# Kernel optimization log

Measured on AMD Instinct MI355X. Metric: run time of the kernel, lower is better.

The kernel has to match this reference:

```python
import jax, jax.numpy as jnp
import numpy as np

IN = 128; HID = 128; OUT = 128; HEADS = 3; T1 = 0.2; T2 = 0.2
B = 512; L = 32; V = 100000; NMETA = 5


def _corr_full(s, t):
    # s, t: (B, L, E, N). Full cross-correlation along last axis.
    # Matches F.conv1d(hs, ht, groups=BLE, padding=N-1): out[k] = sum_m s[k+m-(N-1)] * t[m]
    N = s.shape[-1]
    sp = jnp.pad(s, ((0, 0), (0, 0), (0, 0), (N - 1, N - 1)))
    out = jnp.stack([(sp[..., k:k + N] * t).sum(-1) for k in range(2 * N - 1)], axis=-1)
    return jnp.swapaxes(out, -1, -2)  # (B, L, 2N-1, E)


def _node_att(h, Wt, Ws, Wc):
    # h: (B, L, P, E); Wt/Ws/Wc: (HEADS, E, HID)
    Bh, Lh, P, E = h.shape
    H = h.reshape(Bh * Lh, P, E)
    hi = jnp.einsum('ne,heo->hno', H[:, 0], Wt)                 # target-node projection
    logits = jnp.einsum('npe,heo,hno->hnp', H, Ws, hi) / T1     # (heads, BL, P)
    alpha = jax.nn.softmax(logits, axis=-1)                     # softmax over path positions
    Z = jnp.einsum('hnp,npe,heo->no', alpha, H, Wc) / HEADS     # mean over heads
    return Z.reshape(Bh, Lh, -1)


def _forward(emb_user, emb_item, emb_attr1, emb_attr2, emb_attr3, Wt, Ws, Wc,
             pw1, pb1, pw2, fw1, fb1, fw2, fb2,
             UI, IU, UIUI, IUIU, UIAI1, IAIU1, UIAI2, IAIU2, UIAI3, IAIU3):
    src = emb_user[UI[:, 0, 0]]
    tgt = emb_item[IU[:, 0, 0]]
    ui = jnp.stack([emb_user[UI[..., 0]], emb_item[UI[..., 1]]], axis=3)
    iu = jnp.stack([emb_item[IU[..., 0]], emb_user[IU[..., 1]]], axis=3)

    def p4(tabs, idx):
        return jnp.stack([tabs[k][idx[..., k]] for k in range(4)], axis=3)

    uiui = p4([emb_user, emb_item, emb_user, emb_item], UIUI)
    iuiu = p4([emb_item, emb_user, emb_item, emb_user], IUIU)
    uiai1 = p4([emb_user, emb_item, emb_attr1, emb_item], UIAI1)
    iaiu1 = p4([emb_item, emb_attr1, emb_item, emb_user], IAIU1)
    uiai2 = p4([emb_user, emb_item, emb_attr2, emb_item], UIAI2)
    iaiu2 = p4([emb_item, emb_attr2, emb_item, emb_user], IAIU2)
    uiai3 = p4([emb_user, emb_item, emb_attr3, emb_item], UIAI3)
    iaiu3 = p4([emb_item, emb_attr3, emb_item, emb_user], IAIU3)

    user_feats = [ui, uiui, uiai1, uiai2, uiai3]
    item_feats = [iu, iuiu, iaiu1, iaiu2, iaiu3]
    Hs = [_node_att(_corr_full(uf, itf), Wt[m], Ws[m], Wc[m])
          for m, (uf, itf) in enumerate(zip(user_feats, item_feats))]
    Z = jnp.stack(Hs, 1)                        # (B, 5, L, HID)
    z = Z.reshape(Z.shape[0], -1, HID)          # (B, 5L, HID)
    w = jnp.tanh(z @ pw1 + pb1) @ pw2 / T2      # (B, 5L, 1)
    beta = jax.nn.softmax(w, axis=1)
    path_out = (beta * z).sum(1)                # (B, HID)
    x = jnp.concatenate([src, tgt, path_out], axis=1)
    x = jax.nn.relu(x @ fw1 + fb1)              # dropout in eval mode -> identity
    return jax.nn.sigmoid(x @ fw2 + fb2)        # (B, 1)


def setup_inputs() -> dict:
    key = jax.random.key(0)
    ks = jax.random.split(key, 24)

    def idx(k, n):
        return jax.random.randint(k, (B, L, n), 0, V, dtype=jnp.int32)

    d = {
        'UI': idx(ks[0], 2), 'IU': idx(ks[1], 2),
        'UIUI': idx(ks[2], 4), 'IUIU': idx(ks[3], 4),
        'UIAI1': idx(ks[4], 4), 'IAIU1': idx(ks[5], 4),
        'UIAI2': idx(ks[6], 4), 'IAIU2': idx(ks[7], 4),
        'UIAI3': idx(ks[8], 4), 'IAIU3': idx(ks[9], 4),
    }

    def emb(k):
        t = jax.random.normal(k, (V + 1, IN), jnp.float32) * 0.05
        return t.at[0].set(0.0)  # padding_idx=0

    d['emb_user'] = emb(ks[10]); d['emb_item'] = emb(ks[11])
    d['emb_attr1'] = emb(ks[12]); d['emb_attr2'] = emb(ks[13]); d['emb_attr3'] = emb(ks[14])
    s = (2.0 / (IN + HID)) ** 0.5  # xavier scale
    d['Wt'] = jax.random.normal(ks[15], (NMETA, HEADS, IN, HID), jnp.float32) * s
    d['Ws'] = jax.random.normal(ks[16], (NMETA, HEADS, IN, HID), jnp.float32) * s
    d['Wc'] = jax.random.normal(ks[17], (NMETA, HEADS, IN, HID), jnp.float32) * s
    d['pw1'] = jax.random.normal(ks[18], (HID, HID), jnp.float32) * s
    d['pb1'] = jnp.zeros((HID,), jnp.float32)
    d['pw2'] = jax.random.normal(ks[19], (HID, 1), jnp.float32) * s
    d['fw1'] = jax.random.normal(ks[20], (3 * HID, OUT), jnp.float32) * 0.02
    d['fb1'] = jnp.zeros((OUT,), jnp.float32)
    d['fw2'] = jax.random.normal(ks[21], (OUT, 1), jnp.float32) * 0.02
    d['fb2'] = jnp.zeros((1,), jnp.float32)
    return d


def reference(UI, IU, UIUI, IUIU, UIAI1, IAIU1, UIAI2, IAIU2, UIAI3, IAIU3,
              emb_user, emb_item, emb_attr1, emb_attr2, emb_attr3,
              Wt, Ws, Wc, pw1, pb1, pw2, fw1, fb1, fw2, fb2):
    return _forward(emb_user, emb_item, emb_attr1, emb_attr2, emb_attr3, Wt, Ws, Wc,
                    pw1, pb1, pw2, fw1, fb1, fw2, fb2,
                    UI, IU, UIUI, IUIU, UIAI1, IAIU1, UIAI2, IAIU2, UIAI3, IAIU3)
```

## Files before the change

### kernel.cpp

```cpp
#include <hip/hip_runtime.h>
#include <hip/hip_bf16.h>
#include <cstdint>
#include <cstddef>


typedef __hip_bfloat16 bf16;
typedef __attribute__((ext_vector_type(8))) short  bfrag;
typedef __attribute__((ext_vector_type(4))) float  ffrag;

#define NNODES 16384

__device__ __forceinline__ float bflo(uint32_t u) { return __uint_as_float(u << 16); }
__device__ __forceinline__ float bfhi(uint32_t u) { return __uint_as_float(u & 0xffff0000u); }
__device__ __forceinline__ float bfs(short s) {
  return __uint_as_float(((uint32_t)(unsigned short)s) << 16);
}
__device__ __forceinline__ uint16_t f2bfu(float x) {
  bf16 h = __float2bfloat16(x);
  return *(uint16_t*)&h;
}
__device__ __forceinline__ uint32_t pk2(float lo, float hi) {
  return (uint32_t)f2bfu(lo) | ((uint32_t)f2bfu(hi) << 16);
}

__global__ __launch_bounds__(256) void prep_all(
    const float* __restrict__ Ws, const float* __restrict__ Wt,
    const float* __restrict__ Wc, const float* __restrict__ pw1,
    bf16* __restrict__ BmT, bf16* __restrict__ WcT, bf16* __restrict__ pw1T)
{
  int bid = blockIdx.x;
  int tid = threadIdx.x;
  if (bid < 240) {
    int mh = bid >> 4;
    int g  = bid & 15;
    int m = mh / 3, h = mh % 3;
    const float* ws = Ws + (size_t)mh * 16384;
    const float* wt = Wt + (size_t)mh * 16384;
    int e = tid & 127, half = tid >> 7;
    __shared__ float wtl[2][128];
    for (int ep0 = g * 8; ep0 < g * 8 + 8; ep0 += 2) {
      int ep = ep0 + half;
      wtl[half][e] = wt[ep * 128 + e];
      __syncthreads();
      float acc = 0.f;
      #pragma unroll 4
      for (int o = 0; o < 128; ++o) acc += ws[e * 128 + o] * wtl[half][o];
      BmT[((size_t)(m * 384 + h * 128 + e)) * 128 + ep] = __float2bfloat16(acc);
      __syncthreads();
    }
  } else if (bid < 1200) {
    int idx = (bid - 240) * 256 + tid;
    int he = idx % 384, mo = idx / 384;
    int m = mo >> 7, o = mo & 127;
    WcT[idx] = __float2bfloat16(Wc[((size_t)m * 384 + he) * 128 + o]);
  } else {
    int idx = (bid - 1200) * 256 + tid;
    int o = idx >> 7, k = idx & 127;
    pw1T[idx] = __float2bfloat16(pw1[(size_t)k * 128 + o]);
  }
}

template <int P>
__device__ __forceinline__ void metapath_body(
    char* smem,
    const float* __restrict__ Tu0, const float* __restrict__ Tu1,
    const float* __restrict__ Tu2, const float* __restrict__ Tu3,
    const float* __restrict__ Tt0, const float* __restrict__ Tt1,
    const float* __restrict__ Tt2, const float* __restrict__ Tt3,
    const int* __restrict__ idxU, const int* __restrict__ idxT,
    const bf16* __restrict__ BmT,
    const bf16* __restrict__ WcT,
    bf16* __restrict__ Zall, int m, int tile)
{
  constexpr int PP = 2 * P - 1;
  constexpr int NS = PP * 136;
  bf16* Hs = (bf16*)smem;
  bf16* Ss = Hs + 16 * NS;
  bf16* Al = Ss + 16 * 392;

  int tid = threadIdx.x;
  int lane = tid & 63, wid = tid >> 6;
  int l15 = lane & 15, l4 = lane >> 4;
  int n0 = tile * 16;

  {
    const float* TU[4] = {Tu0, Tu1, Tu2, Tu3};
    const float* TT[4] = {Tt0, Tt1, Tt2, Tt3};
    int e = tid & 127;
    float su[4][P], st[4][P];
    #pragma unroll
    for (int g = 0; g < 4; ++g) {
      int n = n0 + g * 4 + (tid >> 7);
      #pragma unroll
      for (int p = 0; p < P; ++p) {
        su[g][p] = TU[p][(size_t)idxU[n * P + p] * 128 + e];
        st[g][p] = TT[p][(size_t)idxT[n * P + p] * 128 + e];
      }
    }
    #pragma unroll
    for (int g = 0; g < 4; ++g) {
      int ln = g * 4 + (tid >> 7);
      bf16* Hn = &Hs[ln * NS + e];
      #pragma unroll
      for (int k = 0; k < PP; ++k) {
        float acc = 0.f;
        #pragma unroll
        for (int i = 0; i < P; ++i) {
          int j = k + i - (P - 1);
          if (j >= 0 && j < P) acc += su[g][j] * st[g][i];
        }
        Hn[k * 136] = __float2bfloat16(acc);
      }
    }
  }
  __syncthreads();

  {
    bfrag a[4];
    #pragma unroll
    for (int kk = 0; kk < 4; ++kk)
      a[kk] = *(const bfrag*)&Hs[l15 * NS + kk * 32 + 8 * l4];
    #pragma unroll
    for (int f = 0; f < 3; ++f) {
      int col = wid * 48 + f * 16 + l15;
      ffrag acc = {0.f, 0.f, 0.f, 0.f};
      #pragma unroll
      for (int kk = 0; kk < 4; ++kk) {
        bfrag b = *(const bfrag*)&BmT[(size_t)col * 128 + kk * 32 + 8 * l4];
        acc = __builtin_amdgcn_mfma_f32_16x16x32_bf16(a[kk], b, acc, 0, 0, 0);
      }
      #pragma unroll
      for (int r = 0; r < 4; ++r) {
        int node = 4 * l4 + r;
        Ss[node * 392 + col] = __float2bfloat16(acc[r]);
      }
    }
  }
  __syncthreads();

  {
    int nd0 = wid * 2, nd1 = nd0 + 1;
    bool hi = (l15 >= 8);
    int nodeA = hi ? nd1 : nd0;
    int r15 = hi ? (l15 - 8) : l15;
    int ah = (r15 < 3) ? r15 : 2;
    int bp = (r15 < PP) ? r15 : (PP - 1);
    ffrag lacc = {0.f, 0.f, 0.f, 0.f};
    #pragma unroll
    for (int kk = 0; kk < 4; ++kk) {
      bfrag av = *(const bfrag*)&Ss[nodeA * 392 + ah * 128 + kk * 32 + 8 * l4];
      bfrag bv = *(const bfrag*)&Hs[nodeA * NS + bp * 136 + kk * 32 + 8 * l4];
      lacc = __builtin_amdgcn_mfma_f32_16x16x32_bf16(av, bv, lacc, 0, 0, 0);
    }
    bool val = ((l4 == 0) && !hi && (l15 < PP)) ||
               ((l4 == 2) &&  hi && (r15 < PP));
    float lg0 = val ? lacc[0] * 5.0f : -1e30f;
    float lg1 = val ? lacc[1] * 5.0f : -1e30f;
    float lg2 = val ? lacc[2] * 5.0f : -1e30f;
    float m0 = lg0, m1 = lg1, m2 = lg2;
    #pragma unroll
    for (int d = 1; d < 8; d <<= 1) {
      m0 = fmaxf(m0, __shfl_xor(m0, d));
      m1 = fmaxf(m1, __shfl_xor(m1, d));
      m2 = fmaxf(m2, __shfl_xor(m2, d));
    }
    float e0 = val ? __expf(lg0 - m0) : 0.f;
    float e1 = val ? __expf(lg1 - m1) : 0.f;
    float e2 = val ? __expf(lg2 - m2) : 0.f;
    float s0 = e0, s1 = e1, s2 = e2;
    #pragma unroll
    for (int d = 1; d < 8; d <<= 1) {
      s0 += __shfl_xor(s0, d);
      s1 += __shfl_xor(s1, d);
      s2 += __shfl_xor(s2, d);
    }
    if (val) {
      bf16* Aln = Al + nodeA * 24;
      Aln[r15]      = __float2bfloat16(e0 / s0);
      Aln[8 + r15]  = __float2bfloat16(e1 / s1);
      Aln[16 + r15] = __float2bfloat16(e2 / s2);
    }

    int node = tid >> 5, q = tid & 31;
    bfrag al0 = *(const bfrag*)&Al[node * 24];
    bfrag al1 = *(const bfrag*)&Al[node * 24 + 8];
    bfrag al2 = *(const bfrag*)&Al[node * 24 + 16];
    #pragma unroll
    for (int j = 0; j < 2; ++j) {
      int e2i = 4 * q + 2 * j;
      float a00 = 0.f, a01 = 0.f, a10 = 0.f, a11 = 0.f, a20 = 0.f, a21 = 0.f;
      #pragma unroll
      for (int pp = 0; pp < PP; ++pp) {
        uint32_t hv = *(const uint32_t*)&Hs[node * NS + pp * 136 + e2i];
        float lo = bflo(hv), hh = bfhi(hv);
        float f0 = bfs(al0[pp]);
        float f1 = bfs(al1[pp]);
        float f2 = bfs(al2[pp]);
        a00 += f0 * lo; a01 += f0 * hh;
        a10 += f1 * lo; a11 += f1 * hh;
        a20 += f2 * lo; a21 += f2 * hh;
      }
      *(uint32_t*)&Ss[node * 392 +       e2i] = pk2(a00, a01);
      *(uint32_t*)&Ss[node * 392 + 128 + e2i] = pk2(a10, a11);
      *(uint32_t*)&Ss[node * 392 + 256 + e2i] = pk2(a20, a21);
    }
  }
  __syncthreads();

  {
    bfrag a[12];
    #pragma unroll
    for (int kk = 0; kk < 12; ++kk)
      a[kk] = *(const bfrag*)&Ss[l15 * 392 + kk * 32 + 8 * l4];
    int col = wid * 16 + l15;
    ffrag acc = {0.f, 0.f, 0.f, 0.f};
    #pragma unroll
    for (int kk = 0; kk < 12; ++kk) {
      bfrag b = *(const bfrag*)&WcT[(size_t)col * 384 + kk * 32 + 8 * l4];
      acc = __builtin_amdgcn_mfma_f32_16x16x32_bf16(a[kk], b, acc, 0, 0, 0);
    }
    #pragma unroll
    for (int r = 0; r < 4; ++r) {
      int gn = n0 + 4 * l4 + r;
      int crow = (((gn >> 5) * 5 + m) << 5) + (gn & 31);
      Zall[(size_t)crow * 128 + col] = __float2bfloat16(acc[r] * (1.0f / 3.0f));
    }
  }
}

__global__ __launch_bounds__(512) void fused_all(
    const float* __restrict__ emb_user, const float* __restrict__ emb_item,
    const float* __restrict__ emb_a1, const float* __restrict__ emb_a2,
    const float* __restrict__ emb_a3,
    const int* __restrict__ UI,    const int* __restrict__ IU,
    const int* __restrict__ UIUI,  const int* __restrict__ IUIU,
    const int* __restrict__ UIAI1, const int* __restrict__ IAIU1,
    const int* __restrict__ UIAI2, const int* __restrict__ IAIU2,
    const int* __restrict__ UIAI3, const int* __restrict__ IAIU3,
    const bf16* __restrict__ BmT, const bf16* __restrict__ WcT,
    bf16* __restrict__ Zall)
{
  extern __shared__ char smem[];
  int bid = blockIdx.x;
  int m = bid >> 10, tile = bid & 1023;
  if (m == 0) {
    metapath_body<2>(smem, emb_user, emb_item, nullptr, nullptr,
                     emb_item, emb_user, nullptr, nullptr,
                     UI, IU, BmT, WcT, Zall, 0, tile);
  } else {
    const float* u2 = (m == 1) ? emb_user : (m == 2) ? emb_a1
                    : (m == 3) ? emb_a2 : emb_a3;
    const int* iu_ = (m == 1) ? UIUI : (m == 2) ? UIAI1
                   : (m == 3) ? UIAI2 : UIAI3;
    const int* it_ = (m == 1) ? IUIU : (m == 2) ? IAIU1
                   : (m == 3) ? IAIU2 : IAIU3;
    metapath_body<4>(smem, emb_user, emb_item, u2, emb_item,
                     emb_item, u2, emb_item, emb_user,
                     iu_, it_,
                     BmT + (size_t)m * 49152, WcT + (size_t)m * 49152,
                     Zall, m, tile);
  }
}

__global__ __launch_bounds__(512) void fused_tail(
    const bf16* __restrict__ Zall,
    const bf16* __restrict__ pw1T,
    const float* __restrict__ pb1, const float* __restrict__ pw2,
    const int* __restrict__ UI, const int* __restrict__ IU,
    const float* __restrict__ emb_user, const float* __restrict__ emb_item,
    const float* __restrict__ fw1, const float* __restrict__ fb1,
    const float* __restrict__ fw2, const float* __restrict__ fb2,
    float* __restrict__ out)
{
  __shared__ bf16 Zs[160 * 136];
  __shared__ float wrow[160];
  __shared__ float ph[4][128];
  __shared__ float xs[384];
  __shared__ float sred[16];
  __shared__ float yred[2];

  int b = blockIdx.x, tid = threadIdx.x;
  int lane = tid & 63, wid = tid >> 6;
  int l15 = lane & 15, l4 = lane >> 4;

  {
    const float4* src = (const float4*)(Zall + (size_t)b * 160 * 128);
    float4 v[5];
    #pragma unroll
    for (int i = 0; i < 5; ++i) v[i] = src[i * 512 + tid];
    #pragma unroll
    for (int i = 0; i < 5; ++i) {
      int idx = i * 512 + tid;
      int row = idx >> 4, c8 = idx & 15;
      *(float4*)&Zs[row * 136 + c8 * 8] = v[i];
    }
  }
  __syncthreads();

  for (int rf = wid; rf < 10; rf += 8) {
    bfrag a[4];
    #pragma unroll
    for (int kk = 0; kk < 4; ++kk)
      a[kk] = *(const bfrag*)&Zs[(rf * 16 + l15) * 136 + kk * 32 + 8 * l4];
    float part[4] = {0.f, 0.f, 0.f, 0.f};
    #pragma unroll
    for (int f = 0; f < 8; ++f) {
      int col = f * 16 + l15;
      ffrag acc = {0.f, 0.f, 0.f, 0.f};
      #pragma unroll
      for (int kk = 0; kk < 4; ++kk) {
        bfrag bv = *(const bfrag*)&pw1T[(size_t)col * 128 + kk * 32 + 8 * l4];
        acc = __builtin_amdgcn_mfma_f32_16x16x32_bf16(a[kk], bv, acc, 0, 0, 0);
      }
      float bias = pb1[col], w2 = pw2[col];
      #pragma unroll
      for (int r = 0; r < 4; ++r) part[r] += tanhf(acc[r] + bias) * w2;
    }
    #pragma unroll
    for (int d = 1; d < 16; d <<= 1) {
      #pragma unroll
      for (int r = 0; r < 4; ++r) part[r] += __shfl_xor(part[r], d);
    }
    if (l15 == 0) {
      #pragma unroll
      for (int r = 0; r < 4; ++r)
        wrow[rf * 16 + 4 * l4 + r] = part[r] * 5.0f;
    }
  }
  __syncthreads();

  {
    float v = (tid < 160) ? wrow[tid] : -1e30f;
    #pragma unroll
    for (int off = 32; off; off >>= 1) v = fmaxf(v, __shfl_xor(v, off));
    if (lane == 0) sred[wid] = v;
    __syncthreads();
    if (tid < 64) {
      float mval = (lane < 8) ? sred[lane] : -1e30f;
      #pragma unroll
      for (int off = 4; off; off >>= 1) mval = fmaxf(mval, __shfl_xor(mval, off));
      if (lane == 0) sred[8] = mval;
    }
    __syncthreads();
    float mx = sred[8];
    float ev = (tid < 160) ? __expf(wrow[tid] - mx) : 0.f;
    float s = ev;
    #pragma unroll
    for (int off = 32; off; off >>= 1) s += __shfl_xor(s, off);
    if (lane == 0) sred[wid] = s;
    __syncthreads();
    if (tid < 64) {
      float sval = (lane < 8) ? sred[lane] : 0.f;
      #pragma unroll
      for (int off = 4; off; off >>= 1) sval += __shfl_xor(sval, off);
      if (lane == 0) sred[9] = sval;
    }
    __syncthreads();
    if (tid < 160) wrow[tid] = ev / sred[9];
  }
  __syncthreads();

  {
    int e = tid & 127, q = tid >> 7;
    float acc = 0.f;
    #pragma unroll 4
    for (int j = q * 40; j < q * 40 + 40; ++j)
      acc += wrow[j] * __bfloat162float(Zs[j * 136 + e]);
    ph[q][e] = acc;
  }
  __syncthreads();

  {
    int su = UI[b * 64];
    int ti = IU[b * 64];
    if (tid < 128) {
      xs[256 + tid] = ph[0][tid] + ph[1][tid] + ph[2][tid] + ph[3][tid];
    } else if (tid < 256) {
      xs[tid - 128] = emb_user[(size_t)su * 128 + (tid - 128)];
    } else if (tid < 384) {
      xs[tid - 128] = emb_item[(size_t)ti * 128 + (tid - 256)];
    }
  }
  __syncthreads();

  {
    int o = tid & 127, q = tid >> 7;
    float acc = 0.f;
    #pragma unroll 4
    for (int i = q * 96; i < q * 96 + 96; ++i)
      acc += xs[i] * fw1[(size_t)i * 128 + o];
    __syncthreads();
    ph[q][o] = acc;
  }
  __syncthreads();
  if (tid < 128) {
    float y = fmaxf(ph[0][tid] + ph[1][tid] + ph[2][tid] + ph[3][tid] + fb1[tid],
                    0.0f) * fw2[tid];
    #pragma unroll
    for (int off = 32; off; off >>= 1) y += __shfl_down(y, off);
    if ((tid & 63) == 0) yred[tid >> 6] = y;
  }
  __syncthreads();
  if (tid == 0) {
    float s = yred[0] + yred[1] + fb2[0];
    out[b] = 1.0f / (1.0f + expf(-s));
  }
}

extern "C" void kernel_launch(void* const* d_in, const int* in_sizes, int n_in,
                              void* d_out, int out_size, void* d_ws, size_t ws_size,
                              hipStream_t stream)
{
  const int* UI    = (const int*)d_in[0];
  const int* IU    = (const int*)d_in[1];
  const int* UIUI  = (const int*)d_in[2];
  const int* IUIU  = (const int*)d_in[3];
  const int* UIAI1 = (const int*)d_in[4];
  const int* IAIU1 = (const int*)d_in[5];
  const int* UIAI2 = (const int*)d_in[6];
  const int* IAIU2 = (const int*)d_in[7];
  const int* UIAI3 = (const int*)d_in[8];
  const int* IAIU3 = (const int*)d_in[9];
  const float* emb_user = (const float*)d_in[10];
  const float* emb_item = (const float*)d_in[11];
  const float* emb_a1   = (const float*)d_in[12];
  const float* emb_a2   = (const float*)d_in[13];
  const float* emb_a3   = (const float*)d_in[14];
  const float* Wt  = (const float*)d_in[15];
  const float* Ws  = (const float*)d_in[16];
  const float* Wc  = (const float*)d_in[17];
  const float* pw1 = (const float*)d_in[18];
  const float* pb1 = (const float*)d_in[19];
  const float* pw2 = (const float*)d_in[20];
  const float* fw1 = (const float*)d_in[21];
  const float* fb1 = (const float*)d_in[22];
  const float* fw2 = (const float*)d_in[23];
  const float* fb2 = (const float*)d_in[24];
  float* out = (float*)d_out;

  char* wsb = (char*)d_ws;
  bf16*  BmT  = (bf16*)wsb;
  bf16*  WcT  = (bf16*)(wsb + 491520);
  bf16*  pw1T = (bf16*)(wsb + 983040);
  bf16*  Zall = (bf16*)(wsb + 1015808);

  prep_all<<<1264, 256, 0, stream>>>(Ws, Wt, Wc, pw1, BmT, WcT, pw1T);

  fused_all<<<5120, 512, 43776, stream>>>(
      emb_user, emb_item, emb_a1, emb_a2, emb_a3,
      UI, IU, UIUI, IUIU, UIAI1, IAIU1, UIAI2, IAIU2, UIAI3, IAIU3,
      BmT, WcT, Zall);

  fused_tail<<<512, 512, 0, stream>>>(Zall, pw1T, pb1, pw2,
                                      UI, IU, emb_user, emb_item,
                                      fw1, fb1, fw2, fb2, out);
}
```

Baseline: 201.8 us.

## Gather bf16 copies of user/item tables and fuse semantic scoring into main kernel

Adds a pre-pass kernel that converts the user and item embedding tables to bf16 on every call. The main metapath kernel then gathers half-width rows for those tables, while the attribute tables stay fp32. The main kernel also computes the per-row semantic-attention score (pw1 projection, tanh, pw2 dot) right after producing each Z tile, writing it to a buffer, so the tail kernel no longer runs that MFMA pass. The trade-off is a full streaming read and write of two large tables every call, plus extra rounding of the embeddings before the correlation.

```diff
diff --git a/kernel.cpp b/kernel.cpp
--- a/kernel.cpp
+++ b/kernel.cpp
@@ -8,12 +8,10 @@
 typedef __attribute__((ext_vector_type(8))) short  bfrag;
 typedef __attribute__((ext_vector_type(4))) float  ffrag;
 
-#define NNODES 16384
-
 __device__ __forceinline__ float bflo(uint32_t u) { return __uint_as_float(u << 16); }
 __device__ __forceinline__ float bfhi(uint32_t u) { return __uint_as_float(u & 0xffff0000u); }
-__device__ __forceinline__ float bfs(short s) {
-  return __uint_as_float(((uint32_t)(unsigned short)s) << 16);
+__device__ __forceinline__ float bfs(unsigned short s) {
+  return __uint_as_float(((uint32_t)s) << 16);
 }
 __device__ __forceinline__ uint16_t f2bfu(float x) {
   bf16 h = __float2bfloat16(x);
@@ -21,6 +19,22 @@
 }
 __device__ __forceinline__ uint32_t pk2(float lo, float hi) {
   return (uint32_t)f2bfu(lo) | ((uint32_t)f2bfu(hi) << 16);
+}
+
+__global__ __launch_bounds__(256) void conv_emb(
+    const float* __restrict__ a, const float* __restrict__ b,
+    ushort* __restrict__ da, ushort* __restrict__ db, int n4)
+{
+  int stride = gridDim.x * 256;
+  for (int i = blockIdx.x * 256 + threadIdx.x; i < 2 * n4; i += stride) {
+    const float4* s; ushort* d; int j;
+    if (i < n4) { s = (const float4*)a; d = da; j = i; }
+    else        { s = (const float4*)b; d = db; j = i - n4; }
+    float4 v = s[j];
+    ushort4 o;
+    o.x = f2bfu(v.x); o.y = f2bfu(v.y); o.z = f2bfu(v.z); o.w = f2bfu(v.w);
+    ((ushort4*)d)[j] = o;
+  }
 }
 
 __global__ __launch_bounds__(256) void prep_all(
@@ -60,23 +74,24 @@
   }
 }
 
-template <int P>
+template <int P, int UM, int TM>
 __device__ __forceinline__ void metapath_body(
     char* smem,
-    const float* __restrict__ Tu0, const float* __restrict__ Tu1,
-    const float* __restrict__ Tu2, const float* __restrict__ Tu3,
-    const float* __restrict__ Tt0, const float* __restrict__ Tt1,
-    const float* __restrict__ Tt2, const float* __restrict__ Tt3,
+    const void* Tu0, const void* Tu1, const void* Tu2, const void* Tu3,
+    const void* Tt0, const void* Tt1, const void* Tt2, const void* Tt3,
     const int* __restrict__ idxU, const int* __restrict__ idxT,
     const bf16* __restrict__ BmT,
     const bf16* __restrict__ WcT,
-    bf16* __restrict__ Zall, int m, int tile)
+    const bf16* __restrict__ pw1T,
+    const float* __restrict__ pb1, const float* __restrict__ pw2,
+    bf16* __restrict__ Zall, float* __restrict__ wbuf, int m, int tile)
 {
   constexpr int PP = 2 * P - 1;
   constexpr int NS = PP * 136;
   bf16* Hs = (bf16*)smem;
   bf16* Ss = Hs + 16 * NS;
   bf16* Al = Ss + 16 * 392;
+  float* wred = (float*)(Al + 16 * 24);
 
   int tid = threadIdx.x;
   int lane = tid & 63, wid = tid >> 6;
@@ -84,8 +99,8 @@
   int n0 = tile * 16;
 
   {
-    const float* TU[4] = {Tu0, Tu1, Tu2, Tu3};
-    const float* TT[4] = {Tt0, Tt1, Tt2, Tt3};
+    const void* TU[4] = {Tu0, Tu1, Tu2, Tu3};
+    const void* TT[4] = {Tt0, Tt1, Tt2, Tt3};
     int e = tid & 127;
     float su[4][P], st[4][P];
     #pragma unroll
@@ -93,8 +108,12 @@
       int n = n0 + g * 4 + (tid >> 7);
       #pragma unroll
       for (int p = 0; p < P; ++p) {
-        su[g][p] = TU[p][(size_t)idxU[n * P + p] * 128 + e];
-        st[g][p] = TT[p][(size_t)idxT[n * P + p] * 128 + e];
+        size_t ou = (size_t)idxU[n * P + p] * 128 + e;
+        size_t ot = (size_t)idxT[n * P + p] * 128 + e;
+        su[g][p] = ((UM >> p) & 1) ? ((const float*)TU[p])[ou]
+                                   : bfs(((const ushort*)TU[p])[ou]);
+        st[g][p] = ((TM >> p) & 1) ? ((const float*)TT[p])[ot]
+                                   : bfs(((const ushort*)TT[p])[ot]);
       }
     }
     #pragma unroll
@@ -193,9 +212,9 @@
       for (int pp = 0; pp < PP; ++pp) {
         uint32_t hv = *(const uint32_t*)&Hs[node * NS + pp * 136 + e2i];
         float lo = bflo(hv), hh = bfhi(hv);
-        float f0 = bfs(al0[pp]);
-        float f1 = bfs(al1[pp]);
-        float f2 = bfs(al2[pp]);
+        float f0 = bfs((unsigned short)al0[pp]);
+        float f1 = bfs((unsigned short)al1[pp]);
+        float f2 = bfs((unsigned short)al2[pp]);
         a00 += f0 * lo; a01 += f0 * hh;
         a10 += f1 * lo; a11 += f1 * hh;
         a20 += f2 * lo; a21 += f2 * hh;
@@ -207,6 +226,7 @@
   }
   __syncthreads();
 
+  bf16* Zs = Hs;
   {
     bfrag a[12];
     #pragma unroll
@@ -221,15 +241,55 @@
     }
     #pragma unroll
     for (int r = 0; r < 4; ++r) {
-      int gn = n0 + 4 * l4 + r;
+      int node = 4 * l4 + r;
+      int gn = n0 + node;
       int crow = (((gn >> 5) * 5 + m) << 5) + (gn & 31);
-      Zall[(size_t)crow * 128 + col] = __float2bfloat16(acc[r] * (1.0f / 3.0f));
-    }
+      bf16 zb = __float2bfloat16(acc[r] * (1.0f / 3.0f));
+      Zall[(size_t)crow * 128 + col] = zb;
+      Zs[node * 136 + col] = zb;
+    }
+  }
+  __syncthreads();
+
+  {
+    bfrag a5[4];
+    #pragma unroll
+    for (int kk = 0; kk < 4; ++kk)
+      a5[kk] = *(const bfrag*)&Zs[l15 * 136 + kk * 32 + 8 * l4];
+    int col = wid * 16 + l15;
+    ffrag acc5 = {0.f, 0.f, 0.f, 0.f};
+    #pragma unroll
+    for (int kk = 0; kk < 4; ++kk) {
+      bfrag b = *(const bfrag*)&pw1T[(size_t)col * 128 + kk * 32 + 8 * l4];
+      acc5 = __builtin_amdgcn_mfma_f32_16x16x32_bf16(a5[kk], b, acc5, 0, 0, 0);
+    }
+    float bias = pb1[col], w2 = pw2[col];
+    float part[4];
+    #pragma unroll
+    for (int r = 0; r < 4; ++r) part[r] = tanhf(acc5[r] + bias) * w2;
+    #pragma unroll
+    for (int d = 1; d < 16; d <<= 1) {
+      #pragma unroll
+      for (int r = 0; r < 4; ++r) part[r] += __shfl_xor(part[r], d);
+    }
+    if (l15 == 0) {
+      #pragma unroll
+      for (int r = 0; r < 4; ++r) wred[wid * 16 + 4 * l4 + r] = part[r];
+    }
+  }
+  __syncthreads();
+  if (tid < 16) {
+    float s = 0.f;
+    #pragma unroll
+    for (int w = 0; w < 8; ++w) s += wred[w * 16 + tid];
+    int gn = n0 + tid;
+    int crow = (((gn >> 5) * 5 + m) << 5) + (gn & 31);
+    wbuf[crow] = s * 5.0f;
   }
 }
 
 __global__ __launch_bounds__(512) void fused_all(
-    const float* __restrict__ emb_user, const float* __restrict__ emb_item,
+    const ushort* __restrict__ EU, const ushort* __restrict__ EI,
     const float* __restrict__ emb_a1, const float* __restrict__ emb_a2,
     const float* __restrict__ emb_a3,
     const int* __restrict__ UI,    const int* __restrict__ IU,
@@ -238,34 +298,39 @@
     const int* __restrict__ UIAI2, const int* __restrict__ IAIU2,
     const int* __restrict__ UIAI3, const int* __restrict__ IAIU3,
     const bf16* __restrict__ BmT, const bf16* __restrict__ WcT,
-    bf16* __restrict__ Zall)
+    const bf16* __restrict__ pw1T,
+    const float* __restrict__ pb1, const float* __restrict__ pw2,
+    bf16* __restrict__ Zall, float* __restrict__ wbuf)
 {
   extern __shared__ char smem[];
   int bid = blockIdx.x;
   int m = bid >> 10, tile = bid & 1023;
   if (m == 0) {
-    metapath_body<2>(smem, emb_user, emb_item, nullptr, nullptr,
-                     emb_item, emb_user, nullptr, nullptr,
-                     UI, IU, BmT, WcT, Zall, 0, tile);
+    metapath_body<2, 0, 0>(smem, EU, EI, nullptr, nullptr,
+                           EI, EU, nullptr, nullptr,
+                           UI, IU, BmT, WcT, pw1T, pb1, pw2,
+                           Zall, wbuf, 0, tile);
+  } else if (m == 1) {
+    metapath_body<4, 0, 0>(smem, EU, EI, EU, EI,
+                           EI, EU, EI, EU,
+                           UIUI, IUIU,
+                           BmT + (size_t)1 * 49152, WcT + (size_t)1 * 49152,
+                           pw1T, pb1, pw2, Zall, wbuf, 1, tile);
   } else {
-    const float* u2 = (m == 1) ? emb_user : (m == 2) ? emb_a1
-                    : (m == 3) ? emb_a2 : emb_a3;
-    const int* iu_ = (m == 1) ? UIUI : (m == 2) ? UIAI1
-                   : (m == 3) ? UIAI2 : UIAI3;
-    const int* it_ = (m == 1) ? IUIU : (m == 2) ? IAIU1
-                   : (m == 3) ? IAIU2 : IAIU3;
-    metapath_body<4>(smem, emb_user, emb_item, u2, emb_item,
-                     emb_item, u2, emb_item, emb_user,
-                     iu_, it_,
-                     BmT + (size_t)m * 49152, WcT + (size_t)m * 49152,
-                     Zall, m, tile);
+    const float* at = (m == 2) ? emb_a1 : (m == 3) ? emb_a2 : emb_a3;
+    const int* iu_ = (m == 2) ? UIAI1 : (m == 3) ? UIAI2 : UIAI3;
+    const int* it_ = (m == 2) ? IAIU1 : (m == 3) ? IAIU2 : IAIU3;
+    metapath_body<4, 4, 2>(smem, EU, EI, at, EI,
+                           EI, at, EI, EU,
+                           iu_, it_,
+                           BmT + (size_t)m * 49152, WcT + (size_t)m * 49152,
+                           pw1T, pb1, pw2, Zall, wbuf, m, tile);
   }
 }
 
 __global__ __launch_bounds__(512) void fused_tail(
     const bf16* __restrict__ Zall,
-    const bf16* __restrict__ pw1T,
-    const float* __restrict__ pb1, const float* __restrict__ pw2,
+    const float* __restrict__ wbuf,
     const int* __restrict__ UI, const int* __restrict__ IU,
     const float* __restrict__ emb_user, const float* __restrict__ emb_item,
     const float* __restrict__ fw1, const float* __restrict__ fb1,
@@ -281,50 +346,18 @@
 
   int b = blockIdx.x, tid = threadIdx.x;
   int lane = tid & 63, wid = tid >> 6;
-  int l15 = lane & 15, l4 = lane >> 4;
 
   {
     const float4* src = (const float4*)(Zall + (size_t)b * 160 * 128);
     float4 v[5];
     #pragma unroll
     for (int i = 0; i < 5; ++i) v[i] = src[i * 512 + tid];
+    if (tid < 160) wrow[tid] = wbuf[b * 160 + tid];
     #pragma unroll
     for (int i = 0; i < 5; ++i) {
       int idx = i * 512 + tid;
       int row = idx >> 4, c8 = idx & 15;
       *(float4*)&Zs[row * 136 + c8 * 8] = v[i];
-    }
-  }
-  __syncthreads();
-
-  for (int rf = wid; rf < 10; rf += 8) {
-    bfrag a[4];
-    #pragma unroll
-    for (int kk = 0; kk < 4; ++kk)
-      a[kk] = *(const bfrag*)&Zs[(rf * 16 + l15) * 136 + kk * 32 + 8 * l4];
-    float part[4] = {0.f, 0.f, 0.f, 0.f};
-    #pragma unroll
-    for (int f = 0; f < 8; ++f) {
-      int col = f * 16 + l15;
-      ffrag acc = {0.f, 0.f, 0.f, 0.f};
-      #pragma unroll
-      for (int kk = 0; kk < 4; ++kk) {
-        bfrag bv = *(const bfrag*)&pw1T[(size_t)col * 128 + kk * 32 + 8 * l4];
-        acc = __builtin_amdgcn_mfma_f32_16x16x32_bf16(a[kk], bv, acc, 0, 0, 0);
-      }
-      float bias = pb1[col], w2 = pw2[col];
-      #pragma unroll
-      for (int r = 0; r < 4; ++r) part[r] += tanhf(acc[r] + bias) * w2;
-    }
-    #pragma unroll
-    for (int d = 1; d < 16; d <<= 1) {
-      #pragma unroll
-      for (int r = 0; r < 4; ++r) part[r] += __shfl_xor(part[r], d);
-    }
-    if (l15 == 0) {
-      #pragma unroll
-      for (int r = 0; r < 4; ++r)
-        wrow[rf * 16 + 4 * l4 + r] = part[r] * 5.0f;
     }
   }
   __syncthreads();
@@ -439,19 +472,24 @@
   float* out = (float*)d_out;
 
   char* wsb = (char*)d_ws;
-  bf16*  BmT  = (bf16*)wsb;
-  bf16*  WcT  = (bf16*)(wsb + 491520);
-  bf16*  pw1T = (bf16*)(wsb + 983040);
-  bf16*  Zall = (bf16*)(wsb + 1015808);
-
+  bf16*   BmT  = (bf16*)wsb;
+  bf16*   WcT  = (bf16*)(wsb + 491520);
+  bf16*   pw1T = (bf16*)(wsb + 983040);
+  bf16*   Zall = (bf16*)(wsb + 1015808);
+  float*  wbuf = (float*)(wsb + 21987328);
+  ushort* EU16 = (ushort*)(wsb + 22315008);
+  ushort* EI16 = (ushort*)(wsb + 47915264);
+
+  int n4 = (100001 * 128) / 4;
+  conv_emb<<<8192, 256, 0, stream>>>(emb_user, emb_item, EU16, EI16, n4);
   prep_all<<<1264, 256, 0, stream>>>(Ws, Wt, Wc, pw1, BmT, WcT, pw1T);
 
-  fused_all<<<5120, 512, 43776, stream>>>(
-      emb_user, emb_item, emb_a1, emb_a2, emb_a3,
+  fused_all<<<5120, 512, 44288, stream>>>(
+      EU16, EI16, emb_a1, emb_a2, emb_a3,
       UI, IU, UIUI, IUIU, UIAI1, IAIU1, UIAI2, IAIU2, UIAI3, IAIU3,
-      BmT, WcT, Zall);
-
-  fused_tail<<<512, 512, 0, stream>>>(Zall, pw1T, pb1, pw2,
+      BmT, WcT, pw1T, pb1, pw2, Zall, wbuf);
+
+  fused_tail<<<512, 512, 0, stream>>>(Zall, wbuf,
                                       UI, IU, emb_user, emb_item,
                                       fw1, fb1, fw2, fb2, out);
 }
```

Result: slower. 225.7 us (+11.8%).
